# Kernel optimization log

Measured on AMD Instinct MI355X. Metric: run time of the kernel, lower is better.

## Reference

```python
import jax, jax.numpy as jnp
import numpy as np

BETA = 0.25


def setup_inputs() -> dict:
    key = jax.random.key(0)
    k1, k2 = jax.random.split(key)
    z = jax.random.normal(k1, (16, 1024, 256), dtype=jnp.float32)
    embedding = jax.random.normal(k2, (8192, 256), dtype=jnp.float32)
    return {"z": z, "embedding": embedding}


def reference(z, embedding):
    e_dim = embedding.shape[-1]
    z_flat = jnp.reshape(z, (-1, e_dim))  # [N, e_dim]
    # d[i,k] = ||z_i||^2 + ||e_k||^2 - 2 z_i . e_k  -> [N, n_e]
    d = (jnp.sum(z_flat ** 2, axis=1, keepdims=True)
         + jnp.sum(embedding ** 2, axis=1)
         - 2.0 * jnp.einsum('nd,kd->nk', z_flat, embedding))
    min_encoding_indices = jnp.argmin(d, axis=1)  # [N]
    z_q = embedding[min_encoding_indices]
    z_q = jnp.reshape(z_q, z.shape)
    loss = (jnp.mean((jax.lax.stop_gradient(z_q) - z) ** 2)
            + BETA * jnp.mean((z_q - jax.lax.stop_gradient(z)) ** 2))
    z_q = z + jax.lax.stop_gradient(z_q - z)  # straight-through estimator
    return (z_q, loss, min_encoding_indices)
```

## Files before the change

### kernel.cpp

```cpp
#include <hip/hip_runtime.h>
#include <stdint.h>

#define N_ROWS   16384
#define DIM      256
#define N_CODES  8192
#define ZQ_ELEMS 4194304

typedef _Float16 f16x8 __attribute__((ext_vector_type(8)));
typedef _Float16 f16x4 __attribute__((ext_vector_type(4)));
typedef float    f32x16 __attribute__((ext_vector_type(16)));
typedef unsigned long long u64;

#define WS_ET  0
#define WS_PK  (8519680)

static __device__ __forceinline__ u64 packkey(float d, int c) {
    unsigned int u = __float_as_uint(d);
    u ^= ((unsigned int)((int)u >> 31)) | 0x80000000u;
    return ((u64)u << 32) | (unsigned int)c;
}

__global__ void vq_prep(const float* __restrict__ emb, _Float16* __restrict__ et,
                        u64* __restrict__ pkeys, float* __restrict__ loss_ptr) {
    __shared__ _Float16 sh[2][32][272];
    const int t = threadIdx.x, w = t >> 6, l = t & 63;
    if (blockIdx.x == 0 && t == 0) *loss_ptr = 0.0f;
    if (t < 64) pkeys[blockIdx.x * 64 + t] = ~0ULL;
    const int code0 = blockIdx.x * 32;
    #pragma unroll
    for (int j = 0; j < 8; ++j) {
        const int cl = w * 8 + j;
        float4 v = *(const float4*)(emb + (size_t)(code0 + cl) * DIM + l * 4);
        float xs[4] = {v.x, v.y, v.z, v.w};
        f16x4 hh, lo;
        float s = 0.0f;
        #pragma unroll
        for (int i = 0; i < 4; ++i) {
            _Float16 h = (_Float16)xs[i];
            hh[i] = h;
            lo[i] = (_Float16)(xs[i] - (float)h);
            s += xs[i] * xs[i];
        }
        *(f16x4*)&sh[0][cl][l * 4] = hh;
        *(f16x4*)&sh[1][cl][l * 4] = lo;
        #pragma unroll
        for (int off = 32; off > 0; off >>= 1) s += __shfl_down(s, off, 64);
        if (l == 0) {
            _Float16 nh = (_Float16)s;
            _Float16 nl = (_Float16)(s - (float)nh);
            f16x8 aug;
            #pragma unroll
            for (int i = 0; i < 8; ++i) aug[i] = (_Float16)0;
            aug[0] = nh; aug[1] = nl;
            *(f16x8*)(et + ((size_t)524288 + code0 + cl) * 8) = aug;
        }
    }
    __syncthreads();
    #pragma unroll
    for (int pp = 0; pp < 8; ++pp) {
        const int gi = pp * 256 + t;
        const int p = gi >> 10, ks = (gi >> 6) & 15, cl = (gi >> 1) & 31, h = gi & 1;
        f16x8 frag = *(const f16x8*)&sh[p][cl][ks * 16 + h * 8];
        const size_t unit = (size_t)p * 262144 + (size_t)ks * 16384
                          + (size_t)(code0 + cl) * 2 + h;
        *(f16x8*)(et + unit * 8) = frag;
    }
}

__global__ __launch_bounds__(512, 2)
void vq_main(const float* __restrict__ z, const _Float16* __restrict__ et,
             u64* __restrict__ pkeys) {
    extern __shared__ char smem[];
    u64* run = (u64*)(smem + 133120);

    const int tid = threadIdx.x;
    const int w = tid >> 6, L = tid & 63, lo5 = L & 31, hi1 = L >> 5;
    const int rb = blockIdx.x >> 2, sp = blockIdx.x & 3;
    const int row0 = rb * 128, codeS = sp * 2048;

    const float* zr = z + (size_t)row0 * DIM;
    #pragma unroll
    for (int jj = 0; jj < 16; ++jj) {
        const int idx = jj * 512 + tid;
        const int r = idx >> 6, q = idx & 63;
        float4 v = *(const float4*)(zr + (size_t)r * DIM + q * 4);
        float xs[4] = {v.x, v.y, v.z, v.w};
        f16x4 hh, lo;
        #pragma unroll
        for (int i = 0; i < 4; ++i) {
            const float m2 = -2.0f * xs[i];
            _Float16 h = (_Float16)m2;
            hh[i] = h;
            lo[i] = (_Float16)(m2 - (float)h);
        }
        char* base = smem + r * 1040 + q * 8;
        *(f16x4*)(base) = hh;
        *(f16x4*)(base + 512) = lo;
    }
    run[tid] = ~0ULL;
    run[tid + 512] = ~0ULL;

    f16x8 bz;
    #pragma unroll
    for (int i = 0; i < 8; ++i) bz[i] = (_Float16)0;
    if (hi1 == 0) { bz[0] = (_Float16)1; bz[1] = (_Float16)1; }

    f32x16 zacc;
    #pragma unroll
    for (int e = 0; e < 16; ++e) zacc[e] = 0.0f;

    const f16x8* eb  = (const f16x8*)et;
    const f16x8* ebL = eb + 262144;
    const int laneU = lo5 * 2 + hi1;
    const char* zbA = smem + (lo5 * 1040 + hi1 * 16);
    const char* zbB = zbA + 66560;

    f16x8 paug[2];
    {
        const int c0 = codeS + w * 64;
        paug[0] = eb[(size_t)524288 + c0 + lo5];
        paug[1] = eb[(size_t)524288 + c0 + 32 + lo5];
    }
    __syncthreads();

    for (int ci = 0; ci < 4; ++ci) {
        const int c0 = codeS + ci * 512 + w * 64;
        f32x16 acc[2][4];

        __builtin_amdgcn_s_setprio(1);
        #pragma unroll
        for (int mt = 0; mt < 2; ++mt)
            #pragma unroll
            for (int nt = 0; nt < 4; ++nt)
                acc[mt][nt] = __builtin_amdgcn_mfma_f32_32x32x16_f16(paug[mt], bz, zacc, 0, 0, 0);
        __builtin_amdgcn_s_setprio(0);

        if (ci < 3) {
            const int c1 = codeS + (ci + 1) * 512 + w * 64;
            paug[0] = eb[(size_t)524288 + c1 + lo5];
            paug[1] = eb[(size_t)524288 + c1 + 32 + lo5];
        }

        const size_t cu = (size_t)c0 * 2 + laneU;
        #pragma unroll 4
        for (int ksg = 0; ksg < 16; ++ksg) {
            const size_t ub = (size_t)ksg * 16384 + cu;
            f16x8 ah[2], al[2];
            ah[0] = eb[ub];       ah[1] = eb[ub + 64];
            al[0] = ebL[ub];      al[1] = ebL[ub + 64];
            f16x8 bh[4], bl[4];
            #pragma unroll
            for (int nt = 0; nt < 4; ++nt) {
                const char* zp = (nt < 2) ? zbA : zbB;
                bh[nt] = *(const f16x8*)(zp + (ksg * 32 + (nt & 1) * 33280));
                bl[nt] = *(const f16x8*)(zp + (ksg * 32 + (nt & 1) * 33280 + 512));
            }
            __builtin_amdgcn_s_setprio(1);
            #pragma unroll
            for (int mt = 0; mt < 2; ++mt)
                #pragma unroll
                for (int nt = 0; nt < 4; ++nt) {
                    acc[mt][nt] = __builtin_amdgcn_mfma_f32_32x32x16_f16(ah[mt], bh[nt], acc[mt][nt], 0, 0, 0);
                    acc[mt][nt] = __builtin_amdgcn_mfma_f32_32x32x16_f16(ah[mt], bl[nt], acc[mt][nt], 0, 0, 0);
                    acc[mt][nt] = __builtin_amdgcn_mfma_f32_32x32x16_f16(al[mt], bh[nt], acc[mt][nt], 0, 0, 0);
                }
            __builtin_amdgcn_s_setprio(0);
        }

        #pragma unroll
        for (int nt = 0; nt < 4; ++nt) {
            float mm[16];
            #pragma unroll
            for (int r = 0; r < 16; ++r)
                mm[r] = fminf(acc[0][nt][r], acc[1][nt][r]);
            #pragma unroll
            for (int s2 = 8; s2 > 0; s2 >>= 1)
                #pragma unroll
                for (int r = 0; r < 8; ++r)
                    if (r < s2) mm[r] = fminf(mm[r], mm[r + s2]);
            const float m = mm[0];
            int rel = 64;
            #pragma unroll
            for (int mt = 0; mt < 2; ++mt)
                #pragma unroll
                for (int r = 0; r < 16; ++r) {
                    const int rc = mt * 32 + (r & 3) + 8 * (r >> 2);
                    const int cand = (acc[mt][nt][r] == m) ? rc : 64;
                    rel = cand < rel ? cand : rel;
                }
            u64 best = packkey(m, c0 + 4 * hi1 + rel);
            const u64 o = __shfl_xor(best, 32, 64);
            if (o < best) best = o;
            if (hi1 == 0) {
                u64* p = &run[w * 128 + nt * 32 + lo5];
                if (best < *p) *p = best;
            }
        }
    }

    __syncthreads();
    if (tid < 128) {
        u64 k = run[tid];
        #pragma unroll
        for (int w2 = 1; w2 < 8; ++w2) { u64 o = run[w2 * 128 + tid]; if (o < k) k = o; }
        atomicMin(&pkeys[row0 + tid], k);
    }
}

__global__ __launch_bounds__(512)
void vq_final(const float* __restrict__ z, const float* __restrict__ emb,
              const u64* __restrict__ pkeys,
              float* __restrict__ zq_out, float* __restrict__ loss_out,
              float* __restrict__ idx_out) {
    __shared__ int best[64];
    const int t = threadIdx.x;
    const int row0 = blockIdx.x * 64;
    if (t < 64) {
        const u64 k = pkeys[row0 + t];
        const int code = (int)(k & 0xFFFFFFFFu);
        best[t] = code;
        idx_out[row0 + t] = (float)code;
    }
    __syncthreads();
    const int wave = t >> 6, lane = t & 63;
    float lsum = 0.0f;
    #pragma unroll
    for (int rr = 0; rr < 8; ++rr) {
        const int rl = wave * 8 + rr;
        const int rg = row0 + rl;
        const int code = best[rl];
        float4 ev = *(const float4*)(emb + (size_t)code * DIM + lane * 4);
        float4 zv = *(const float4*)(z   + (size_t)rg   * DIM + lane * 4);
        float dx = ev.x - zv.x, dy = ev.y - zv.y;
        float dz = ev.z - zv.z, dw = ev.w - zv.w;
        lsum += dx * dx + dy * dy + dz * dz + dw * dw;
        *(float4*)(zq_out + (size_t)rg * DIM + lane * 4) = ev;
    }
    #pragma unroll
    for (int off = 32; off > 0; off >>= 1) lsum += __shfl_down(lsum, off, 64);
    if (lane == 0) atomicAdd(loss_out, lsum * (1.25f / (float)ZQ_ELEMS));
}

extern "C" void kernel_launch(void* const* d_in, const int* in_sizes, int n_in,
                              void* d_out, int out_size, void* d_ws, size_t ws_size,
                              hipStream_t stream) {
    const float* z   = (const float*)d_in[0];
    const float* emb = (const float*)d_in[1];
    float* out  = (float*)d_out;
    float* zq   = out;
    float* loss = out + ZQ_ELEMS;
    float* idx  = out + ZQ_ELEMS + 1;

    char* ws = (char*)d_ws;
    _Float16* et = (_Float16*)(ws + WS_ET);
    u64*   pk    = (u64*)(ws + WS_PK);

    static bool attr_set = false;
    if (!attr_set) {
        hipFuncSetAttribute((const void*)vq_main,
                            hipFuncAttributeMaxDynamicSharedMemorySize, 141312);
        attr_set = true;
    }

    vq_prep<<<256, 256, 0, stream>>>(emb, et, pk, loss);
    vq_main<<<512, 512, 141312, stream>>>(z, et, pk);
    vq_final<<<N_ROWS / 64, 512, 0, stream>>>(z, emb, pk, zq, loss, idx);
}
```

Baseline: 276.9 us.

## Prefetch next k-step codebook fragments in registers and regroup layout per split

```diff
diff --git a/kernel.cpp b/kernel.cpp
--- a/kernel.cpp
+++ b/kernel.cpp
@@ -27,6 +27,7 @@
     if (blockIdx.x == 0 && t == 0) *loss_ptr = 0.0f;
     if (t < 64) pkeys[blockIdx.x * 64 + t] = ~0ULL;
     const int code0 = blockIdx.x * 32;
+    const int sp0 = code0 >> 11, cw0 = code0 & 2047;
     #pragma unroll
     for (int j = 0; j < 8; ++j) {
         const int cl = w * 8 + j;
@@ -61,8 +62,8 @@
         const int gi = pp * 256 + t;
         const int p = gi >> 10, ks = (gi >> 6) & 15, cl = (gi >> 1) & 31, h = gi & 1;
         f16x8 frag = *(const f16x8*)&sh[p][cl][ks * 16 + h * 8];
-        const size_t unit = (size_t)p * 262144 + (size_t)ks * 16384
-                          + (size_t)(code0 + cl) * 2 + h;
+        const size_t unit = (size_t)p * 262144 + (size_t)sp0 * 65536
+                          + (size_t)ks * 4096 + (size_t)(cw0 + cl) * 2 + h;
         *(f16x8*)(et + unit * 8) = frag;
     }
 }
@@ -112,6 +113,7 @@
     const f16x8* eb  = (const f16x8*)et;
     const f16x8* ebL = eb + 262144;
     const int laneU = lo5 * 2 + hi1;
+    const size_t spB = (size_t)sp * 65536;
     const char* zbA = smem + (lo5 * 1040 + hi1 * 16);
     const char* zbB = zbA + 66560;
 
@@ -121,10 +123,16 @@
         paug[0] = eb[(size_t)524288 + c0 + lo5];
         paug[1] = eb[(size_t)524288 + c0 + 32 + lo5];
     }
+    f16x8 aC0, aC1, aC2, aC3;
+    {
+        const size_t cu = spB + (size_t)(w * 64) * 2 + laneU;
+        aC0 = eb[cu]; aC1 = eb[cu + 64]; aC2 = ebL[cu]; aC3 = ebL[cu + 64];
+    }
     __syncthreads();
 
     for (int ci = 0; ci < 4; ++ci) {
         const int c0 = codeS + ci * 512 + w * 64;
+        const size_t cu = spB + (size_t)(ci * 512 + w * 64) * 2 + laneU;
         f32x16 acc[2][4];
 
         __builtin_amdgcn_s_setprio(1);
@@ -141,30 +149,58 @@
             paug[1] = eb[(size_t)524288 + c1 + 32 + lo5];
         }
 
-        const size_t cu = (size_t)c0 * 2 + laneU;
         #pragma unroll 4
         for (int ksg = 0; ksg < 16; ++ksg) {
-            const size_t ub = (size_t)ksg * 16384 + cu;
-            f16x8 ah[2], al[2];
-            ah[0] = eb[ub];       ah[1] = eb[ub + 64];
-            al[0] = ebL[ub];      al[1] = ebL[ub + 64];
-            f16x8 bh[4], bl[4];
-            #pragma unroll
-            for (int nt = 0; nt < 4; ++nt) {
-                const char* zp = (nt < 2) ? zbA : zbB;
-                bh[nt] = *(const f16x8*)(zp + (ksg * 32 + (nt & 1) * 33280));
-                bl[nt] = *(const f16x8*)(zp + (ksg * 32 + (nt & 1) * 33280 + 512));
+            const size_t ubn = cu + (size_t)(ksg + 1) * 4096;
+            f16x8 aN0 = eb[ubn], aN1 = eb[ubn + 64];
+            f16x8 aN2 = ebL[ubn], aN3 = ebL[ubn + 64];
+
+            {
+                f16x8 bh0 = *(const f16x8*)(zbA + (ksg * 32));
+                f16x8 bl0 = *(const f16x8*)(zbA + (ksg * 32 + 512));
+                f16x8 bh1 = *(const f16x8*)(zbA + (ksg * 32 + 33280));
+                f16x8 bl1 = *(const f16x8*)(zbA + (ksg * 32 + 33280 + 512));
+                __builtin_amdgcn_s_setprio(1);
+                acc[0][0] = __builtin_amdgcn_mfma_f32_32x32x16_f16(aC0, bh0, acc[0][0], 0, 0, 0);
+                acc[0][0] = __builtin_amdgcn_mfma_f32_32x32x16_f16(aC0, bl0, acc[0][0], 0, 0, 0);
+                acc[0][0] = __builtin_amdgcn_mfma_f32_32x32x16_f16(aC2, bh0, acc[0][0], 0, 0, 0);
+                acc[0][1] = __builtin_amdgcn_mfma_f32_32x32x16_f16(aC0, bh1, acc[0][1], 0, 0, 0);
+                acc[0][1] = __builtin_amdgcn_mfma_f32_32x32x16_f16(aC0, bl1, acc[0][1], 0, 0, 0);
+                acc[0][1] = __builtin_amdgcn_mfma_f32_32x32x16_f16(aC2, bh1, acc[0][1], 0, 0, 0);
+                acc[1][0] = __builtin_amdgcn_mfma_f32_32x32x16_f16(aC1, bh0, acc[1][0], 0, 0, 0);
+                acc[1][0] = __builtin_amdgcn_mfma_f32_32x32x16_f16(aC1, bl0, acc[1][0], 0, 0, 0);
+                acc[1][0] = __builtin_amdgcn_mfma_f32_32x32x16_f16(aC3, bh0, acc[1][0], 0, 0, 0);
+                acc[1][1] = __builtin_amdgcn_mfma_f32_32x32x16_f16(aC1, bh1, acc[1][1], 0, 0, 0);
+                acc[1][1] = __builtin_amdgcn_mfma_f32_32x32x16_f16(aC1, bl1, acc[1][1], 0, 0, 0);
+                acc[1][1] = __builtin_amdgcn_mfma_f32_32x32x16_f16(aC3, bh1, acc[1][1], 0, 0, 0);
+                __builtin_amdgcn_s_setprio(0);
             }
-            __builtin_amdgcn_s_setprio(1);
-            #pragma unroll
-            for (int mt = 0; mt < 2; ++mt)
-                #pragma unroll
-                for (int nt = 0; nt < 4; ++nt) {
-                    acc[mt][nt] = __builtin_amdgcn_mfma_f32_32x32x16_f16(ah[mt], bh[nt], acc[mt][nt], 0, 0, 0);
-                    acc[mt][nt] = __builtin_amdgcn_mfma_f32_32x32x16_f16(ah[mt], bl[nt], acc[mt][nt], 0, 0, 0);
-                    acc[mt][nt] = __builtin_amdgcn_mfma_f32_32x32x16_f16(al[mt], bh[nt], acc[mt][nt], 0, 0, 0);
-                }
-            __builtin_amdgcn_s_setprio(0);
+            {
+                f16x8 bh2 = *(const f16x8*)(zbB + (ksg * 32));
+                f16x8 bl2 = *(const f16x8*)(zbB + (ksg * 32 + 512));
+                f16x8 bh3 = *(const f16x8*)(zbB + (ksg * 32 + 33280));
+                f16x8 bl3 = *(const f16x8*)(zbB + (ksg * 32 + 33280 + 512));
+                __builtin_amdgcn_s_setprio(1);
+                acc[0][2] = __builtin_amdgcn_mfma_f32_32x32x16_f16(aC0, bh2, acc[0][2], 0, 0, 0);
+                acc[0][2] = __builtin_amdgcn_mfma_f32_32x32x16_f16(aC0, bl2, acc[0][2], 0, 0, 0);
+                acc[0][2] = __builtin_amdgcn_mfma_f32_32x32x16_f16(aC2, bh2, acc[0][2], 0, 0, 0);
+                acc[0][3] = __builtin_amdgcn_mfma_f32_32x32x16_f16(aC0, bh3, acc[0][3], 0, 0, 0);
+                acc[0][3] = __builtin_amdgcn_mfma_f32_32x32x16_f16(aC0, bl3, acc[0][3], 0, 0, 0);
+                acc[0][3] = __builtin_amdgcn_mfma_f32_32x32x16_f16(aC2, bh3, acc[0][3], 0, 0, 0);
+                acc[1][2] = __builtin_amdgcn_mfma_f32_32x32x16_f16(aC1, bh2, acc[1][2], 0, 0, 0);
+                acc[1][2] = __builtin_amdgcn_mfma_f32_32x32x16_f16(aC1, bl2, acc[1][2], 0, 0, 0);
+                acc[1][2] = __builtin_amdgcn_mfma_f32_32x32x16_f16(aC3, bh2, acc[1][2], 0, 0, 0);
+                acc[1][3] = __builtin_amdgcn_mfma_f32_32x32x16_f16(aC1, bh3, acc[1][3], 0, 0, 0);
+                acc[1][3] = __builtin_amdgcn_mfma_f32_32x32x16_f16(aC1, bl3, acc[1][3], 0, 0, 0);
+                acc[1][3] = __builtin_amdgcn_mfma_f32_32x32x16_f16(aC3, bh3, acc[1][3], 0, 0, 0);
+                __builtin_amdgcn_s_setprio(0);
+            }
+            aC0 = aN0; aC1 = aN1; aC2 = aN2; aC3 = aN3;
+        }
+
+        {
+            const size_t cuN = spB + (size_t)((((ci + 1) & 3) * 512) + w * 64) * 2 + laneU;
+            aC0 = eb[cuN]; aC1 = eb[cuN + 64]; aC2 = ebL[cuN]; aC3 = ebL[cuN + 64];
         }
 
         #pragma unroll
```

New measurement: 274.3 us. No clear change (-0.9%).

## Prefetch fragments, shrink per-wave tile, derive loss from min distance

Applied to the files above, without the earlier changes.

```diff
diff --git a/kernel.cpp b/kernel.cpp
--- a/kernel.cpp
+++ b/kernel.cpp
@@ -19,6 +19,8 @@
     u ^= ((unsigned int)((int)u >> 31)) | 0x80000000u;
     return ((u64)u << 32) | (unsigned int)c;
 }
+
+#define MFMA16(a, b, c) __builtin_amdgcn_mfma_f32_32x32x16_f16((a), (b), (c), 0, 0, 0)
 
 __global__ void vq_prep(const float* __restrict__ emb, _Float16* __restrict__ et,
                         u64* __restrict__ pkeys, float* __restrict__ loss_ptr) {
@@ -27,6 +29,7 @@
     if (blockIdx.x == 0 && t == 0) *loss_ptr = 0.0f;
     if (t < 64) pkeys[blockIdx.x * 64 + t] = ~0ULL;
     const int code0 = blockIdx.x * 32;
+    const int sp0 = code0 >> 11, cw0 = code0 & 2047;
     #pragma unroll
     for (int j = 0; j < 8; ++j) {
         const int cl = w * 8 + j;
@@ -61,8 +64,8 @@
         const int gi = pp * 256 + t;
         const int p = gi >> 10, ks = (gi >> 6) & 15, cl = (gi >> 1) & 31, h = gi & 1;
         f16x8 frag = *(const f16x8*)&sh[p][cl][ks * 16 + h * 8];
-        const size_t unit = (size_t)p * 262144 + (size_t)ks * 16384
-                          + (size_t)(code0 + cl) * 2 + h;
+        const size_t unit = (size_t)p * 262144 + (size_t)sp0 * 65536
+                          + (size_t)ks * 4096 + (size_t)(cw0 + cl) * 2 + h;
         *(f16x8*)(et + unit * 8) = frag;
     }
 }
@@ -72,6 +75,7 @@
              u64* __restrict__ pkeys) {
     extern __shared__ char smem[];
     u64* run = (u64*)(smem + 133120);
+    float* zn = (float*)(smem + 141312);
 
     const int tid = threadIdx.x;
     const int w = tid >> 6, L = tid & 63, lo5 = L & 31, hi1 = L >> 5;
@@ -85,6 +89,7 @@
         const int r = idx >> 6, q = idx & 63;
         float4 v = *(const float4*)(zr + (size_t)r * DIM + q * 4);
         float xs[4] = {v.x, v.y, v.z, v.w};
+        float ss = xs[0]*xs[0] + xs[1]*xs[1] + xs[2]*xs[2] + xs[3]*xs[3];
         f16x4 hh, lo;
         #pragma unroll
         for (int i = 0; i < 4; ++i) {
@@ -96,6 +101,9 @@
         char* base = smem + r * 1040 + q * 8;
         *(f16x4*)(base) = hh;
         *(f16x4*)(base + 512) = lo;
+        #pragma unroll
+        for (int off = 32; off > 0; off >>= 1) ss += __shfl_down(ss, off, 64);
+        if (L == 0) zn[r] = ss;
     }
     run[tid] = ~0ULL;
     run[tid + 512] = ~0ULL;
@@ -112,67 +120,81 @@
     const f16x8* eb  = (const f16x8*)et;
     const f16x8* ebL = eb + 262144;
     const int laneU = lo5 * 2 + hi1;
+    const size_t spB = (size_t)sp * 65536;
     const char* zbA = smem + (lo5 * 1040 + hi1 * 16);
     const char* zbB = zbA + 66560;
 
-    f16x8 paug[2];
+    f16x8 paug = eb[(size_t)524288 + codeS + w * 32 + lo5];
+    f16x8 ahC, alC;
     {
-        const int c0 = codeS + w * 64;
-        paug[0] = eb[(size_t)524288 + c0 + lo5];
-        paug[1] = eb[(size_t)524288 + c0 + 32 + lo5];
-    }
-    __syncthreads();
-
-    for (int ci = 0; ci < 4; ++ci) {
-        const int c0 = codeS + ci * 512 + w * 64;
-        f32x16 acc[2][4];
+        const size_t cu0 = spB + (size_t)(w * 64 + laneU);
+        ahC = eb[cu0]; alC = ebL[cu0];
+    }
+    __syncthreads();
+    f16x8 b0h = *(const f16x8*)(zbA);
+    f16x8 b0l = *(const f16x8*)(zbA + 512);
+    f16x8 b1h = *(const f16x8*)(zbA + 33280);
+    f16x8 b1l = *(const f16x8*)(zbA + 33280 + 512);
+    f16x8 b2h = *(const f16x8*)(zbB);
+    f16x8 b2l = *(const f16x8*)(zbB + 512);
+    f16x8 b3h = *(const f16x8*)(zbB + 33280);
+    f16x8 b3l = *(const f16x8*)(zbB + 33280 + 512);
+
+    for (int ci = 0; ci < 8; ++ci) {
+        const int c0 = codeS + ci * 256 + w * 32;
+        const size_t cu = spB + (size_t)(ci * 512 + w * 64 + laneU);
+        f32x16 acc[4];
 
         __builtin_amdgcn_s_setprio(1);
         #pragma unroll
-        for (int mt = 0; mt < 2; ++mt)
-            #pragma unroll
-            for (int nt = 0; nt < 4; ++nt)
-                acc[mt][nt] = __builtin_amdgcn_mfma_f32_32x32x16_f16(paug[mt], bz, zacc, 0, 0, 0);
+        for (int nt = 0; nt < 4; ++nt)
+            acc[nt] = MFMA16(paug, bz, zacc);
         __builtin_amdgcn_s_setprio(0);
 
-        if (ci < 3) {
-            const int c1 = codeS + (ci + 1) * 512 + w * 64;
-            paug[0] = eb[(size_t)524288 + c1 + lo5];
-            paug[1] = eb[(size_t)524288 + c1 + 32 + lo5];
-        }
-
-        const size_t cu = (size_t)c0 * 2 + laneU;
+        if (ci < 7)
+            paug = eb[(size_t)524288 + c0 + 256 + lo5];
+
         #pragma unroll 4
         for (int ksg = 0; ksg < 16; ++ksg) {
-            const size_t ub = (size_t)ksg * 16384 + cu;
-            f16x8 ah[2], al[2];
-            ah[0] = eb[ub];       ah[1] = eb[ub + 64];
-            al[0] = ebL[ub];      al[1] = ebL[ub + 64];
-            f16x8 bh[4], bl[4];
-            #pragma unroll
-            for (int nt = 0; nt < 4; ++nt) {
-                const char* zp = (nt < 2) ? zbA : zbB;
-                bh[nt] = *(const f16x8*)(zp + (ksg * 32 + (nt & 1) * 33280));
-                bl[nt] = *(const f16x8*)(zp + (ksg * 32 + (nt & 1) * 33280 + 512));
-            }
+            const size_t ubn = (ksg < 15)
+                ? (cu + (size_t)(ksg + 1) * 4096)
+                : (spB + (size_t)((((ci + 1) & 7) * 512) + w * 64 + laneU));
+            f16x8 ahN = eb[ubn], alN = ebL[ubn];
+            const int ko = ((ksg + 1) & 15) * 32;
+            f16x8 b0hN = *(const f16x8*)(zbA + ko);
+            f16x8 b0lN = *(const f16x8*)(zbA + ko + 512);
+            f16x8 b1hN = *(const f16x8*)(zbA + ko + 33280);
+            f16x8 b1lN = *(const f16x8*)(zbA + ko + 33280 + 512);
+            f16x8 b2hN = *(const f16x8*)(zbB + ko);
+            f16x8 b2lN = *(const f16x8*)(zbB + ko + 512);
+            f16x8 b3hN = *(const f16x8*)(zbB + ko + 33280);
+            f16x8 b3lN = *(const f16x8*)(zbB + ko + 33280 + 512);
+
             __builtin_amdgcn_s_setprio(1);
-            #pragma unroll
-            for (int mt = 0; mt < 2; ++mt)
-                #pragma unroll
-                for (int nt = 0; nt < 4; ++nt) {
-                    acc[mt][nt] = __builtin_amdgcn_mfma_f32_32x32x16_f16(ah[mt], bh[nt], acc[mt][nt], 0, 0, 0);
-                    acc[mt][nt] = __builtin_amdgcn_mfma_f32_32x32x16_f16(ah[mt], bl[nt], acc[mt][nt], 0, 0, 0);
-                    acc[mt][nt] = __builtin_amdgcn_mfma_f32_32x32x16_f16(al[mt], bh[nt], acc[mt][nt], 0, 0, 0);
-                }
+            acc[0] = MFMA16(ahC, b0h, acc[0]);
+            acc[0] = MFMA16(ahC, b0l, acc[0]);
+            acc[0] = MFMA16(alC, b0h, acc[0]);
+            acc[1] = MFMA16(ahC, b1h, acc[1]);
+            acc[1] = MFMA16(ahC, b1l, acc[1]);
+            acc[1] = MFMA16(alC, b1h, acc[1]);
+            acc[2] = MFMA16(ahC, b2h, acc[2]);
+            acc[2] = MFMA16(ahC, b2l, acc[2]);
+            acc[2] = MFMA16(alC, b2h, acc[2]);
+            acc[3] = MFMA16(ahC, b3h, acc[3]);
+            acc[3] = MFMA16(ahC, b3l, acc[3]);
+            acc[3] = MFMA16(alC, b3h, acc[3]);
             __builtin_amdgcn_s_setprio(0);
+
+            ahC = ahN; alC = alN;
+            b0h = b0hN; b0l = b0lN; b1h = b1hN; b1l = b1lN;
+            b2h = b2hN; b2l = b2lN; b3h = b3hN; b3l = b3lN;
         }
 
         #pragma unroll
         for (int nt = 0; nt < 4; ++nt) {
             float mm[16];
             #pragma unroll
-            for (int r = 0; r < 16; ++r)
-                mm[r] = fminf(acc[0][nt][r], acc[1][nt][r]);
+            for (int r = 0; r < 16; ++r) mm[r] = acc[nt][r];
             #pragma unroll
             for (int s2 = 8; s2 > 0; s2 >>= 1)
                 #pragma unroll
@@ -181,14 +203,13 @@
             const float m = mm[0];
             int rel = 64;
             #pragma unroll
-            for (int mt = 0; mt < 2; ++mt)
-                #pragma unroll
-                for (int r = 0; r < 16; ++r) {
-                    const int rc = mt * 32 + (r & 3) + 8 * (r >> 2);
-                    const int cand = (acc[mt][nt][r] == m) ? rc : 64;
-                    rel = cand < rel ? cand : rel;
-                }
-            u64 best = packkey(m, c0 + 4 * hi1 + rel);
+            for (int r = 0; r < 16; ++r) {
+                const int rc = (r & 3) + 8 * (r >> 2);
+                const int cand = (acc[nt][r] == m) ? rc : 64;
+                rel = cand < rel ? cand : rel;
+            }
+            const float zrow = zn[nt * 32 + lo5];
+            u64 best = packkey(m + zrow, c0 + 4 * hi1 + rel);
             const u64 o = __shfl_xor(best, 32, 64);
             if (o < best) best = o;
             if (hi1 == 0) {
@@ -207,38 +228,34 @@
     }
 }
 
-__global__ __launch_bounds__(512)
-void vq_final(const float* __restrict__ z, const float* __restrict__ emb,
-              const u64* __restrict__ pkeys,
+__global__ __launch_bounds__(256)
+void vq_final(const float* __restrict__ emb, const u64* __restrict__ pkeys,
               float* __restrict__ zq_out, float* __restrict__ loss_out,
               float* __restrict__ idx_out) {
-    __shared__ int best[64];
+    __shared__ int bestc[64];
     const int t = threadIdx.x;
     const int row0 = blockIdx.x * 64;
     if (t < 64) {
         const u64 k = pkeys[row0 + t];
         const int code = (int)(k & 0xFFFFFFFFu);
-        best[t] = code;
+        unsigned int mu = (unsigned int)(k >> 32);
+        mu = (mu & 0x80000000u) ? (mu ^ 0x80000000u) : ~mu;
+        float d = __uint_as_float(mu);
+        bestc[t] = code;
         idx_out[row0 + t] = (float)code;
+        #pragma unroll
+        for (int off = 32; off > 0; off >>= 1) d += __shfl_down(d, off, 64);
+        if (t == 0) atomicAdd(loss_out, d * (1.25f / (float)ZQ_ELEMS));
     }
     __syncthreads();
     const int wave = t >> 6, lane = t & 63;
-    float lsum = 0.0f;
-    #pragma unroll
-    for (int rr = 0; rr < 8; ++rr) {
-        const int rl = wave * 8 + rr;
-        const int rg = row0 + rl;
-        const int code = best[rl];
+    #pragma unroll
+    for (int rr = 0; rr < 16; ++rr) {
+        const int rl = wave * 16 + rr;
+        const int code = bestc[rl];
         float4 ev = *(const float4*)(emb + (size_t)code * DIM + lane * 4);
-        float4 zv = *(const float4*)(z   + (size_t)rg   * DIM + lane * 4);
-        float dx = ev.x - zv.x, dy = ev.y - zv.y;
-        float dz = ev.z - zv.z, dw = ev.w - zv.w;
-        lsum += dx * dx + dy * dy + dz * dz + dw * dw;
-        *(float4*)(zq_out + (size_t)rg * DIM + lane * 4) = ev;
-    }
-    #pragma unroll
-    for (int off = 32; off > 0; off >>= 1) lsum += __shfl_down(lsum, off, 64);
-    if (lane == 0) atomicAdd(loss_out, lsum * (1.25f / (float)ZQ_ELEMS));
+        *(float4*)(zq_out + (size_t)(row0 + rl) * DIM + lane * 4) = ev;
+    }
 }
 
 extern "C" void kernel_launch(void* const* d_in, const int* in_sizes, int n_in,
@@ -258,11 +275,11 @@
     static bool attr_set = false;
     if (!attr_set) {
         hipFuncSetAttribute((const void*)vq_main,
-                            hipFuncAttributeMaxDynamicSharedMemorySize, 141312);
+                            hipFuncAttributeMaxDynamicSharedMemorySize, 141824);
         attr_set = true;
     }
 
     vq_prep<<<256, 256, 0, stream>>>(emb, et, pk, loss);
-    vq_main<<<512, 512, 141312, stream>>>(z, et, pk);
-    vq_final<<<N_ROWS / 64, 512, 0, stream>>>(z, emb, pk, zq, loss, idx);
-}
+    vq_main<<<512, 512, 141824, stream>>>(z, et, pk);
+    vq_final<<<N_ROWS / 64, 256, 0, stream>>>(emb, pk, zq, loss, idx);
+}
```

New measurement: 262.9 us. 5.1% less time.
